# Optimization experiments

Hardware: AMD Instinct MI355X
Metric: run time of the kernel (lower is better)

The kernel has to match this reference:

```python
import jax, jax.numpy as jnp
import numpy as np

THRESHOLD = 0.5
VARIANCE = (0.1, 0.2)
ALPHA = 0.25
GAMMA = 2
NUM_CLASSES = 2
EPS = 1e-07


def _point_form(p):
    # center-form [cx,cy,w,h] -> corner-form [x0,y0,x1,y1]
    return jnp.concatenate([p[:, :2] - p[:, 2:] / 2, p[:, :2] + p[:, 2:] / 2], axis=1)


def _jaccard(a, b):
    # a: [O,4] corner-form truths, b: [P,4] corner-form priors -> IoU [O,P]
    lt = jnp.maximum(a[:, None, :2], b[None, :, :2])
    rb = jnp.minimum(a[:, None, 2:], b[None, :, 2:])
    wh = jnp.clip(rb - lt, 0.0)
    inter = wh[..., 0] * wh[..., 1]
    area_a = ((a[:, 2] - a[:, 0]) * (a[:, 3] - a[:, 1]))[:, None]
    area_b = ((b[:, 2] - b[:, 0]) * (b[:, 3] - b[:, 1]))[None, :]
    return inter / (area_a + area_b - inter)


def _encode(matched, priors):
    # matched: [P,4] corner-form GT, priors: [P,4] center-form
    g_cxcy = ((matched[:, :2] + matched[:, 2:]) / 2 - priors[:, :2]) / (VARIANCE[0] * priors[:, 2:])
    g_wh = jnp.log((matched[:, 2:] - matched[:, :2]) / priors[:, 2:]) / VARIANCE[1]
    return jnp.concatenate([g_cxcy, g_wh], axis=1)


def _match(truths, labels, priors):
    # truths: [O,4] corner-form, labels: [O], priors: [P,4] center-form
    overlaps = _jaccard(truths, _point_form(priors))            # [O,P]
    best_prior_idx = jnp.argmax(overlaps, axis=1)               # [O]
    best_truth_overlap = jnp.max(overlaps, axis=0)              # [P]
    best_truth_idx = jnp.argmax(overlaps, axis=0)               # [P]
    # guarantee each GT keeps its best prior
    best_truth_overlap = best_truth_overlap.at[best_prior_idx].set(2.0)
    best_truth_idx = best_truth_idx.at[best_prior_idx].set(jnp.arange(truths.shape[0]))
    matched = truths[best_truth_idx]                            # [P,4]
    conf = labels[best_truth_idx].astype(jnp.int32) + 1
    conf = jnp.where(best_truth_overlap < THRESHOLD, 0, conf)   # background -> 0
    loc = _encode(matched, priors)
    return loc, conf


def setup_inputs() -> dict:
    key = jax.random.key(0)
    k1, k2, k3, k4, k5, k6 = jax.random.split(key, 6)
    B, P, O = 128, 24564, 20
    loc_data = jax.random.normal(k1, (B, P, 4), dtype=jnp.float32)
    conf_data = jax.random.normal(k2, (B, P, NUM_CLASSES), dtype=jnp.float32)
    # priors in center-form with valid positive w,h
    cxcy = jax.random.uniform(k3, (P, 2), minval=0.05, maxval=0.95)
    wh = jax.random.uniform(k4, (P, 2), minval=0.05, maxval=0.3)
    priors = jnp.concatenate([cxcy, wh], axis=1).astype(jnp.float32)
    # GT boxes in corner-form + label column (single foreground class 0)
    gc = jax.random.uniform(k5, (B, O, 2), minval=0.15, maxval=0.85)
    gwh = jax.random.uniform(k6, (B, O, 2), minval=0.05, maxval=0.25)
    bbox_targets = jnp.concatenate(
        [gc - gwh / 2, gc + gwh / 2, jnp.zeros((B, O, 1))], axis=-1
    ).astype(jnp.float32)
    return {"loc_data": loc_data, "conf_data": conf_data, "priors": priors,
            "bbox_targets": bbox_targets}


def reference(loc_data, conf_data, priors, bbox_targets):
    # per-image matching, vectorized over the batch
    loc_t, conf_t = jax.vmap(lambda gt: _match(gt[:, :4], gt[:, 4], priors))(bbox_targets)
    loc_t = jax.lax.stop_gradient(loc_t)
    conf_t = jax.lax.stop_gradient(conf_t)

    pos = conf_t > 0                                             # [B,P]
    # smooth-L1 on positives (sum reduction); masking == dynamic gather + sum
    d = loc_data - loc_t
    ad = jnp.abs(d)
    sl1 = jnp.where(ad < 1.0, 0.5 * d * d, ad - 0.5)
    loss_l = jnp.sum(sl1 * pos[..., None].astype(sl1.dtype))

    # focal loss over pos+neg (conf_t > -1); torch one-hot via eye(2)
    pos_neg = conf_t > -1
    t = jax.nn.one_hot(conf_t, NUM_CLASSES, dtype=jnp.float32)   # [B,P,2]
    logit = jnp.clip(jax.nn.softmax(conf_data, axis=-1), EPS, 1.0 - EPS)
    fl = ALPHA * (-t * jnp.log(logit)) * (1.0 - logit) ** GAMMA
    loss_c = jnp.sum(fl * pos_neg[..., None].astype(fl.dtype))

    num_pos = jnp.maximum(1.0, jnp.sum(pos).astype(jnp.float32))
    return loss_l / num_pos, loss_c / num_pos
```

## Files before the change

kernel.cpp:

```cpp
#include <hip/hip_runtime.h>


#define NB 128
#define NP 24564
#define NO 20

#define IPT1 12
#define NCH1 8
#define NBLK1 (NB * NCH1)
#define NPART (NBLK1 + NB)

#define PK_OFF 0
#define PL_OFF ((size_t)NB * NO * 8)
#define PN_OFF (PL_OFF + (size_t)NPART * 8)
#define WS_NEEDED (PN_OFF + (size_t)NPART * 4)

__device__ __forceinline__ float fast_rcp(float x) {
    return __builtin_amdgcn_rcpf(x);
}

__device__ __forceinline__ float focal_term(float2 cd, int conf) {
    float mx = fmaxf(cd.x, cd.y);
    float e0 = __expf(cd.x - mx), e1 = __expf(cd.y - mx);
    if (conf > 1) return 0.0f;
    float pc = ((conf == 0) ? e0 : e1) * fast_rcp(e0 + e1);
    pc = fminf(fmaxf(pc, 1e-7f), 1.0f - 1e-7f);
    float om = 1.0f - pc;
    return 0.25f * (-__logf(pc)) * om * om;
}

__device__ __forceinline__ float sl1_term(float4 m, float4 pr, float4 ld) {
    float gx = ((m.x + m.z) * 0.5f - pr.x) / (0.1f * pr.z);
    float gy = ((m.y + m.w) * 0.5f - pr.y) / (0.1f * pr.w);
    float gw = logf((m.z - m.x) / pr.z) / 0.2f;
    float gh = logf((m.w - m.y) / pr.w) / 0.2f;
    float d0 = ld.x - gx, d1 = ld.y - gy, d2 = ld.z - gw, d3 = ld.w - gh;
    float a0 = fabsf(d0), a1 = fabsf(d1), a2 = fabsf(d2), a3 = fabsf(d3);
    float r = (a0 < 1.0f) ? 0.5f * d0 * d0 : a0 - 0.5f;
    r += (a1 < 1.0f) ? 0.5f * d1 * d1 : a1 - 0.5f;
    r += (a2 < 1.0f) ? 0.5f * d2 * d2 : a2 - 0.5f;
    r += (a3 < 1.0f) ? 0.5f * d3 * d3 : a3 - 0.5f;
    return r;
}

__global__ __launch_bounds__(256) void init_ws_kernel(unsigned long long* __restrict__ packed) {
    int i = blockIdx.x * 256 + threadIdx.x;
    if (i < NB * NO) packed[i] = 0ull;
}

__global__ __launch_bounds__(256) void match_loss_kernel(
    const float4* __restrict__ loc_data,
    const float2* __restrict__ conf_data,
    const float4* __restrict__ priors,
    const float* __restrict__ bbox,
    unsigned long long* __restrict__ packed,
    float2* __restrict__ part_loss,
    unsigned int* __restrict__ part_np)
{
    const int img  = blockIdx.x / NCH1;
    const int base = (blockIdx.x % NCH1) * (256 * IPT1);
    const int tid  = threadIdx.x;

    __shared__ float4 s_truth[NO];
    __shared__ float  s_area[NO];
    __shared__ int    s_label[NO];
    if (tid < NO) {
        const float* t = bbox + ((size_t)img * NO + tid) * 5;
        float4 tb = make_float4(t[0], t[1], t[2], t[3]);
        s_truth[tid] = tb;
        s_area[tid]  = (tb.z - tb.x) * (tb.w - tb.y);
        s_label[tid] = (int)t[4];
    }
    __syncthreads();

    float bf[NO];
    int   bk[NO];
#pragma unroll
    for (int o = 0; o < NO; ++o) { bf[o] = -1.0f; bk[o] = 0; }

    float lossl = 0.0f, lossc = 0.0f;
    int np = 0;

    for (int k = 0; k < IPT1; ++k) {
        const int p = base + k * 256 + tid;
        if (p >= NP) break;

        float4 pr = priors[p];
        float px0 = pr.x - pr.z * 0.5f, py0 = pr.y - pr.w * 0.5f;
        float px1 = pr.x + pr.z * 0.5f, py1 = pr.y + pr.w * 0.5f;
        float parea = (px1 - px0) * (py1 - py0);

        float bestv = -1.0f;
        int bi = 0;
#pragma unroll
        for (int o = 0; o < NO; ++o) {
            float4 tb = s_truth[o];
            float lx = fmaxf(tb.x, px0), ly = fmaxf(tb.y, py0);
            float rx = fminf(tb.z, px1), ry = fminf(tb.w, py1);
            float w = fmaxf(rx - lx, 0.0f);
            float h = fmaxf(ry - ly, 0.0f);
            float inter = w * h;
            float iou = inter * fast_rcp(s_area[o] + parea - inter);
            if (iou > bf[o]) { bf[o] = iou; bk[o] = k; }
            if (iou > bestv) { bestv = iou; bi = o; }
        }

        const int conf = (bestv >= 0.5f) ? (s_label[bi] + 1) : 0;
        if (conf > 0) {
            np++;
            lossl += sl1_term(s_truth[bi], pr, loc_data[(size_t)img * NP + p]);
        }
        lossc += focal_term(conf_data[(size_t)img * NP + p], conf);
    }

#pragma unroll
    for (int o = 0; o < NO; ++o) {
        const int p = base + bk[o] * 256 + tid;
        unsigned long long v = ((unsigned long long)__float_as_uint(bf[o]) << 32)
                             | (unsigned long long)(0xFFFFFFFFu - (unsigned)p);
#pragma unroll
        for (int s = 32; s > 0; s >>= 1) {
            unsigned long long u = __shfl_xor(v, s, 64);
            v = (v > u) ? v : u;
        }
        if ((tid & 63) == 0) atomicMax(&packed[img * NO + o], v);
    }

#pragma unroll
    for (int s = 32; s > 0; s >>= 1) {
        lossl += __shfl_xor(lossl, s, 64);
        lossc += __shfl_xor(lossc, s, 64);
        np    += __shfl_xor(np, s, 64);
    }
    __shared__ float s_ll[4], s_lc[4];
    __shared__ int s_np4[4];
    int wid = tid >> 6;
    if ((tid & 63) == 0) { s_ll[wid] = lossl; s_lc[wid] = lossc; s_np4[wid] = np; }
    __syncthreads();
    if (tid == 0) {
        float tl = 0.0f, tc = 0.0f;
        int tn = 0;
        for (int w = 0; w < 4; ++w) { tl += s_ll[w]; tc += s_lc[w]; tn += s_np4[w]; }
        part_loss[blockIdx.x] = make_float2(tl, tc);
        part_np[blockIdx.x]   = (unsigned int)tn;
    }
}

__global__ __launch_bounds__(64) void fixup_kernel(
    const float4* __restrict__ loc_data,
    const float2* __restrict__ conf_data,
    const float4* __restrict__ priors,
    const float* __restrict__ bbox,
    const unsigned long long* __restrict__ packed,
    float2* __restrict__ part_loss,
    unsigned int* __restrict__ part_np)
{
    const int img = blockIdx.x;
    const int o   = threadIdx.x;

    __shared__ float4 s_truth[NO];
    __shared__ float  s_area[NO];
    __shared__ int    s_label[NO];
    if (o < NO) {
        const float* t = bbox + ((size_t)img * NO + o) * 5;
        float4 tb = make_float4(t[0], t[1], t[2], t[3]);
        s_truth[o] = tb;
        s_area[o]  = (tb.z - tb.x) * (tb.w - tb.y);
        s_label[o] = (int)t[4];
    }
    __syncthreads();

    int bp = -1;
    if (o < NO) {
        unsigned long long v = packed[(size_t)img * NO + o];
        bp = (int)(0xFFFFFFFFu - (unsigned)(v & 0xFFFFFFFFull));
    }
    bool win = (o < NO);
#pragma unroll
    for (int o2 = 0; o2 < NO; ++o2) {
        int bp2 = __shfl(bp, o2, 64);
        if (o2 > o && bp2 == bp) win = false;
    }

    float dll = 0.0f, dlc = 0.0f;
    int dnp = 0;
    if (win) {
        float4 pr = priors[bp];
        float px0 = pr.x - pr.z * 0.5f, py0 = pr.y - pr.w * 0.5f;
        float px1 = pr.x + pr.z * 0.5f, py1 = pr.y + pr.w * 0.5f;
        float parea = (px1 - px0) * (py1 - py0);

        float bestv = -1.0f;
        int bi = 0;
#pragma unroll
        for (int o3 = 0; o3 < NO; ++o3) {
            float4 tb = s_truth[o3];
            float lx = fmaxf(tb.x, px0), ly = fmaxf(tb.y, py0);
            float rx = fminf(tb.z, px1), ry = fminf(tb.w, py1);
            float w = fmaxf(rx - lx, 0.0f);
            float h = fmaxf(ry - ly, 0.0f);
            float inter = w * h;
            float iou = inter * fast_rcp(s_area[o3] + parea - inter);
            if (iou > bestv) { bestv = iou; bi = o3; }
        }
        const int conf_old = (bestv >= 0.5f) ? (s_label[bi] + 1) : 0;
        const int conf_new = s_label[o] + 1;

        float2 cd = conf_data[(size_t)img * NP + bp];
        float4 ld = loc_data[(size_t)img * NP + bp];

        dlc = focal_term(cd, conf_new) - focal_term(cd, conf_old);
        float sl_new = sl1_term(s_truth[o], pr, ld);
        float sl_old = (conf_old > 0) ? sl1_term(s_truth[bi], pr, ld) : 0.0f;
        dll = sl_new - sl_old;
        dnp = (conf_old == 0) ? 1 : 0;
    }

#pragma unroll
    for (int s = 32; s > 0; s >>= 1) {
        dll += __shfl_xor(dll, s, 64);
        dlc += __shfl_xor(dlc, s, 64);
        dnp += __shfl_xor(dnp, s, 64);
    }
    if (o == 0) {
        part_loss[NBLK1 + img] = make_float2(dll, dlc);
        part_np[NBLK1 + img]   = (unsigned int)dnp;
    }
}

__global__ __launch_bounds__(256) void finalize_kernel(
    const float2* __restrict__ part_loss,
    const unsigned int* __restrict__ part_np,
    float* __restrict__ out)
{
    double ll = 0.0, lc = 0.0;
    unsigned int np = 0;
    for (int i = threadIdx.x; i < NPART; i += 256) {
        float2 v = part_loss[i];
        ll += (double)v.x;
        lc += (double)v.y;
        np += part_np[i];
    }
#pragma unroll
    for (int s = 32; s > 0; s >>= 1) {
        ll += __shfl_xor(ll, s, 64);
        lc += __shfl_xor(lc, s, 64);
        np += __shfl_xor(np, s, 64);
    }
    __shared__ double s_ll[4], s_lc[4];
    __shared__ unsigned int s_np4[4];
    int wid = threadIdx.x >> 6;
    if ((threadIdx.x & 63) == 0) { s_ll[wid] = ll; s_lc[wid] = lc; s_np4[wid] = np; }
    __syncthreads();
    if (threadIdx.x == 0) {
        double tl = 0.0, tc = 0.0;
        unsigned int tn = 0;
        for (int w = 0; w < 4; ++w) { tl += s_ll[w]; tc += s_lc[w]; tn += s_np4[w]; }
        double npd = (tn > 0u) ? (double)tn : 1.0;
        out[0] = (float)(tl / npd);
        out[1] = (float)(tc / npd);
    }
}

extern "C" void kernel_launch(void* const* d_in, const int* in_sizes, int n_in,
                              void* d_out, int out_size, void* d_ws, size_t ws_size,
                              hipStream_t stream) {
    const float4* loc_data  = (const float4*)d_in[0];
    const float2* conf_data = (const float2*)d_in[1];
    const float4* priors    = (const float4*)d_in[2];
    const float*  bbox      = (const float*)d_in[3];
    float* out = (float*)d_out;

    unsigned long long* packed = (unsigned long long*)((char*)d_ws + PK_OFF);
    float2* part_loss = (float2*)((char*)d_ws + PL_OFF);
    unsigned int* part_np = (unsigned int*)((char*)d_ws + PN_OFF);

    init_ws_kernel<<<(NB * NO + 255) / 256, 256, 0, stream>>>(packed);
    match_loss_kernel<<<NBLK1, 256, 0, stream>>>(loc_data, conf_data, priors, bbox,
                                                 packed, part_loss, part_np);
    fixup_kernel<<<NB, 64, 0, stream>>>(loc_data, conf_data, priors, bbox,
                                        packed, part_loss, part_np);
    finalize_kernel<<<1, 256, 0, stream>>>(part_loss, part_np, out);
}
```

Measured before the change: 181.7 us.

## Tile priors per thread, drop atomics, merge fixup and finalize into one kernel

The main matching loop now processes 4 priors per thread at once across each truth box, so every shared-memory truth load serves several IoU computations and more independent work is exposed. Per-truth best-prior keys are reduced within each block in shared memory and written per block, replacing the global atomicMax and removing the init kernel. The fixup and finalize kernels are fused into one single-block epilogue that reduces the per-block keys and applies all corrections, which cuts launches from four to two. The cost is a serial fixup loop over 20 truths in 128 threads of a single block, plus more register pressure from the tiling.

Result: slower. 279.9 us (+54.0%).

```diff
diff --git a/kernel.cpp b/kernel.cpp
--- a/kernel.cpp
+++ b/kernel.cpp
@@ -5,15 +5,16 @@
 #define NP 24564
 #define NO 20
 
-#define IPT1 12
+#define TILE 4
+#define NTILE 3
+#define IPT1 (TILE * NTILE)
 #define NCH1 8
+#define CHUNK (256 * IPT1)
 #define NBLK1 (NB * NCH1)
-#define NPART (NBLK1 + NB)
-
-#define PK_OFF 0
-#define PL_OFF ((size_t)NB * NO * 8)
-#define PN_OFF (PL_OFF + (size_t)NPART * 8)
-#define WS_NEEDED (PN_OFF + (size_t)NPART * 4)
+
+#define KEY_OFF 0
+#define PL_OFF  ((size_t)NBLK1 * NO * 8)
+#define PN_OFF  (PL_OFF + (size_t)NBLK1 * 8)
 
 __device__ __forceinline__ float fast_rcp(float x) {
     return __builtin_amdgcn_rcpf(x);
@@ -43,27 +44,24 @@
     return r;
 }
 
-__global__ __launch_bounds__(256) void init_ws_kernel(unsigned long long* __restrict__ packed) {
-    int i = blockIdx.x * 256 + threadIdx.x;
-    if (i < NB * NO) packed[i] = 0ull;
-}
-
 __global__ __launch_bounds__(256) void match_loss_kernel(
     const float4* __restrict__ loc_data,
     const float2* __restrict__ conf_data,
     const float4* __restrict__ priors,
     const float* __restrict__ bbox,
-    unsigned long long* __restrict__ packed,
+    unsigned long long* __restrict__ pb_keys,
     float2* __restrict__ part_loss,
     unsigned int* __restrict__ part_np)
 {
     const int img  = blockIdx.x / NCH1;
-    const int base = (blockIdx.x % NCH1) * (256 * IPT1);
+    const int base = (blockIdx.x % NCH1) * CHUNK;
     const int tid  = threadIdx.x;
 
     __shared__ float4 s_truth[NO];
     __shared__ float  s_area[NO];
     __shared__ int    s_label[NO];
+    __shared__ unsigned long long s_keys[4][NO];
+
     if (tid < NO) {
         const float* t = bbox + ((size_t)img * NO + tid) * 5;
         float4 tb = make_float4(t[0], t[1], t[2], t[3]);
@@ -81,36 +79,56 @@
     float lossl = 0.0f, lossc = 0.0f;
     int np = 0;
 
-    for (int k = 0; k < IPT1; ++k) {
-        const int p = base + k * 256 + tid;
-        if (p >= NP) break;
-
-        float4 pr = priors[p];
-        float px0 = pr.x - pr.z * 0.5f, py0 = pr.y - pr.w * 0.5f;
-        float px1 = pr.x + pr.z * 0.5f, py1 = pr.y + pr.w * 0.5f;
-        float parea = (px1 - px0) * (py1 - py0);
-
-        float bestv = -1.0f;
-        int bi = 0;
+    for (int t = 0; t < NTILE; ++t) {
+        float qx0[TILE], qy0[TILE], qx1[TILE], qy1[TILE], qa[TILE];
+        float bv[TILE];
+        int   bj[TILE];
+#pragma unroll
+        for (int j = 0; j < TILE; ++j) {
+            const int p = base + (t * TILE + j) * 256 + tid;
+            const bool valid = (p < NP);
+            float4 pr = priors[valid ? p : (NP - 1)];
+            float x0 = pr.x - pr.z * 0.5f, y0 = pr.y - pr.w * 0.5f;
+            float x1 = pr.x + pr.z * 0.5f, y1 = pr.y + pr.w * 0.5f;
+            qx0[j] = valid ? x0 : 3.0e18f;
+            qy0[j] = valid ? y0 : 3.0e18f;
+            qx1[j] = valid ? x1 : 3.0e18f;
+            qy1[j] = valid ? y1 : 3.0e18f;
+            qa[j]  = valid ? (x1 - x0) * (y1 - y0) : 0.0f;
+            bv[j] = -1.0f;
+            bj[j] = 0;
+        }
+
 #pragma unroll
         for (int o = 0; o < NO; ++o) {
-            float4 tb = s_truth[o];
-            float lx = fmaxf(tb.x, px0), ly = fmaxf(tb.y, py0);
-            float rx = fminf(tb.z, px1), ry = fminf(tb.w, py1);
-            float w = fmaxf(rx - lx, 0.0f);
-            float h = fmaxf(ry - ly, 0.0f);
-            float inter = w * h;
-            float iou = inter * fast_rcp(s_area[o] + parea - inter);
-            if (iou > bf[o]) { bf[o] = iou; bk[o] = k; }
-            if (iou > bestv) { bestv = iou; bi = o; }
-        }
-
-        const int conf = (bestv >= 0.5f) ? (s_label[bi] + 1) : 0;
-        if (conf > 0) {
-            np++;
-            lossl += sl1_term(s_truth[bi], pr, loc_data[(size_t)img * NP + p]);
-        }
-        lossc += focal_term(conf_data[(size_t)img * NP + p], conf);
+            const float4 tb = s_truth[o];
+            const float  ta = s_area[o];
+#pragma unroll
+            for (int j = 0; j < TILE; ++j) {
+                float lx = fmaxf(tb.x, qx0[j]), ly = fmaxf(tb.y, qy0[j]);
+                float rx = fminf(tb.z, qx1[j]), ry = fminf(tb.w, qy1[j]);
+                float w = fmaxf(rx - lx, 0.0f);
+                float h = fmaxf(ry - ly, 0.0f);
+                float inter = w * h;
+                float iou = inter * fast_rcp(ta + qa[j] - inter);
+                if (iou > bf[o]) { bf[o] = iou; bk[o] = t * TILE + j; }
+                if (iou > bv[j]) { bv[j] = iou; bj[j] = o; }
+            }
+        }
+
+#pragma unroll
+        for (int j = 0; j < TILE; ++j) {
+            const int p = base + (t * TILE + j) * 256 + tid;
+            if (p >= NP) continue;
+            const int conf = (bv[j] >= 0.5f) ? (s_label[bj[j]] + 1) : 0;
+            if (conf > 0) {
+                np++;
+                float4 pr = priors[p];
+                lossl += sl1_term(s_truth[bj[j]], pr,
+                                  loc_data[(size_t)img * NP + p]);
+            }
+            lossc += focal_term(conf_data[(size_t)img * NP + p], conf);
+        }
     }
 
 #pragma unroll
@@ -123,7 +141,7 @@
             unsigned long long u = __shfl_xor(v, s, 64);
             v = (v > u) ? v : u;
         }
-        if ((tid & 63) == 0) atomicMax(&packed[img * NO + o], v);
+        if ((tid & 63) == 0) s_keys[tid >> 6][o] = v;
     }
 
 #pragma unroll
@@ -134,9 +152,18 @@
     }
     __shared__ float s_ll[4], s_lc[4];
     __shared__ int s_np4[4];
-    int wid = tid >> 6;
+    const int wid = tid >> 6;
     if ((tid & 63) == 0) { s_ll[wid] = lossl; s_lc[wid] = lossc; s_np4[wid] = np; }
     __syncthreads();
+
+    if (tid < NO) {
+        unsigned long long m = s_keys[0][tid];
+        for (int w = 1; w < 4; ++w) {
+            unsigned long long u = s_keys[w][tid];
+            m = (m > u) ? m : u;
+        }
+        pb_keys[(size_t)blockIdx.x * NO + tid] = m;
+    }
     if (tid == 0) {
         float tl = 0.0f, tc = 0.0f;
         int tn = 0;
@@ -146,97 +173,90 @@
     }
 }
 
-__global__ __launch_bounds__(64) void fixup_kernel(
+#define TRS 101
+
+__global__ __launch_bounds__(256) void epilogue_kernel(
     const float4* __restrict__ loc_data,
     const float2* __restrict__ conf_data,
     const float4* __restrict__ priors,
     const float* __restrict__ bbox,
-    const unsigned long long* __restrict__ packed,
-    float2* __restrict__ part_loss,
-    unsigned int* __restrict__ part_np)
-{
-    const int img = blockIdx.x;
-    const int o   = threadIdx.x;
-
-    __shared__ float4 s_truth[NO];
-    __shared__ float  s_area[NO];
-    __shared__ int    s_label[NO];
-    if (o < NO) {
-        const float* t = bbox + ((size_t)img * NO + o) * 5;
-        float4 tb = make_float4(t[0], t[1], t[2], t[3]);
-        s_truth[o] = tb;
-        s_area[o]  = (tb.z - tb.x) * (tb.w - tb.y);
-        s_label[o] = (int)t[4];
-    }
-    __syncthreads();
-
-    int bp = -1;
-    if (o < NO) {
-        unsigned long long v = packed[(size_t)img * NO + o];
-        bp = (int)(0xFFFFFFFFu - (unsigned)(v & 0xFFFFFFFFull));
-    }
-    bool win = (o < NO);
-#pragma unroll
-    for (int o2 = 0; o2 < NO; ++o2) {
-        int bp2 = __shfl(bp, o2, 64);
-        if (o2 > o && bp2 == bp) win = false;
-    }
-
-    float dll = 0.0f, dlc = 0.0f;
-    int dnp = 0;
-    if (win) {
-        float4 pr = priors[bp];
-        float px0 = pr.x - pr.z * 0.5f, py0 = pr.y - pr.w * 0.5f;
-        float px1 = pr.x + pr.z * 0.5f, py1 = pr.y + pr.w * 0.5f;
-        float parea = (px1 - px0) * (py1 - py0);
-
-        float bestv = -1.0f;
-        int bi = 0;
-#pragma unroll
-        for (int o3 = 0; o3 < NO; ++o3) {
-            float4 tb = s_truth[o3];
-            float lx = fmaxf(tb.x, px0), ly = fmaxf(tb.y, py0);
-            float rx = fminf(tb.z, px1), ry = fminf(tb.w, py1);
-            float w = fmaxf(rx - lx, 0.0f);
-            float h = fmaxf(ry - ly, 0.0f);
-            float inter = w * h;
-            float iou = inter * fast_rcp(s_area[o3] + parea - inter);
-            if (iou > bestv) { bestv = iou; bi = o3; }
-        }
-        const int conf_old = (bestv >= 0.5f) ? (s_label[bi] + 1) : 0;
-        const int conf_new = s_label[o] + 1;
-
-        float2 cd = conf_data[(size_t)img * NP + bp];
-        float4 ld = loc_data[(size_t)img * NP + bp];
-
-        dlc = focal_term(cd, conf_new) - focal_term(cd, conf_old);
-        float sl_new = sl1_term(s_truth[o], pr, ld);
-        float sl_old = (conf_old > 0) ? sl1_term(s_truth[bi], pr, ld) : 0.0f;
-        dll = sl_new - sl_old;
-        dnp = (conf_old == 0) ? 1 : 0;
-    }
-
-#pragma unroll
-    for (int s = 32; s > 0; s >>= 1) {
-        dll += __shfl_xor(dll, s, 64);
-        dlc += __shfl_xor(dlc, s, 64);
-        dnp += __shfl_xor(dnp, s, 64);
-    }
-    if (o == 0) {
-        part_loss[NBLK1 + img] = make_float2(dll, dlc);
-        part_np[NBLK1 + img]   = (unsigned int)dnp;
-    }
-}
-
-__global__ __launch_bounds__(256) void finalize_kernel(
+    const unsigned long long* __restrict__ pb_keys,
     const float2* __restrict__ part_loss,
     const unsigned int* __restrict__ part_np,
     float* __restrict__ out)
 {
-    double ll = 0.0, lc = 0.0;
-    unsigned int np = 0;
-    for (int i = threadIdx.x; i < NPART; i += 256) {
-        float2 v = part_loss[i];
+    const int tid = threadIdx.x;
+    __shared__ float s_tr[NB * TRS];
+    __shared__ int   s_bp[NB][NO];
+
+    for (int i = tid; i < NB * NO * 5; i += 256) {
+        const int img = i / (NO * 5), f = i % (NO * 5);
+        s_tr[img * TRS + f] = bbox[i];
+    }
+    for (int u = tid; u < NB * NO; u += 256) {
+        const int img = u / NO, o = u - img * NO;
+        unsigned long long m = 0ull;
+        for (int c = 0; c < NCH1; ++c) {
+            unsigned long long v = pb_keys[((size_t)(img * NCH1 + c)) * NO + o];
+            m = (m > v) ? m : v;
+        }
+        s_bp[img][o] = (int)(0xFFFFFFFFu - (unsigned)(m & 0xFFFFFFFFull));
+    }
+    __syncthreads();
+
+    float dll = 0.0f, dlc = 0.0f;
+    int dnp = 0;
+    if (tid < NB) {
+        const int img = tid;
+        for (int o = 0; o < NO; ++o) {
+            const int bp = s_bp[img][o];
+            bool win = true;
+            for (int o2 = o + 1; o2 < NO; ++o2) win = win && (s_bp[img][o2] != bp);
+            if (!win) continue;
+
+            float4 pr = priors[bp];
+            const float px0 = pr.x - pr.z * 0.5f, py0 = pr.y - pr.w * 0.5f;
+            const float px1 = pr.x + pr.z * 0.5f, py1 = pr.y + pr.w * 0.5f;
+            const float parea = (px1 - px0) * (py1 - py0);
+
+            float bestv = -1.0f;
+            int bi = 0;
+            for (int o3 = 0; o3 < NO; ++o3) {
+                const float* tp = &s_tr[img * TRS + o3 * 5];
+                const float tx0 = tp[0], ty0 = tp[1], tx1 = tp[2], ty1 = tp[3];
+                const float ta = (tx1 - tx0) * (ty1 - ty0);
+                float lx = fmaxf(tx0, px0), ly = fmaxf(ty0, py0);
+                float rx = fminf(tx1, px1), ry = fminf(ty1, py1);
+                float w = fmaxf(rx - lx, 0.0f);
+                float h = fmaxf(ry - ly, 0.0f);
+                float inter = w * h;
+                float iou = inter * fast_rcp(ta + parea - inter);
+                if (iou > bestv) { bestv = iou; bi = o3; }
+            }
+            const int conf_old = (bestv >= 0.5f)
+                               ? ((int)s_tr[img * TRS + bi * 5 + 4] + 1) : 0;
+            const int conf_new = (int)s_tr[img * TRS + o * 5 + 4] + 1;
+
+            const float2 cd = conf_data[(size_t)img * NP + bp];
+            const float4 ld = loc_data[(size_t)img * NP + bp];
+
+            dlc += focal_term(cd, conf_new) - focal_term(cd, conf_old);
+            const float* tn_ = &s_tr[img * TRS + o * 5];
+            float sl_new = sl1_term(make_float4(tn_[0], tn_[1], tn_[2], tn_[3]), pr, ld);
+            float sl_old = 0.0f;
+            if (conf_old > 0) {
+                const float* to_ = &s_tr[img * TRS + bi * 5];
+                sl_old = sl1_term(make_float4(to_[0], to_[1], to_[2], to_[3]), pr, ld);
+            }
+            dll += sl_new - sl_old;
+            dnp += (conf_old == 0) ? 1 : 0;
+        }
+    }
+
+    double ll = (double)dll, lc = (double)dlc;
+    unsigned int np = (unsigned int)dnp;
+    for (int i = tid; i < NBLK1; i += 256) {
+        const float2 v = part_loss[i];
         ll += (double)v.x;
         lc += (double)v.y;
         np += part_np[i];
@@ -247,16 +267,16 @@
         lc += __shfl_xor(lc, s, 64);
         np += __shfl_xor(np, s, 64);
     }
-    __shared__ double s_ll[4], s_lc[4];
-    __shared__ unsigned int s_np4[4];
-    int wid = threadIdx.x >> 6;
-    if ((threadIdx.x & 63) == 0) { s_ll[wid] = ll; s_lc[wid] = lc; s_np4[wid] = np; }
+    __shared__ double r_ll[4], r_lc[4];
+    __shared__ unsigned int r_np[4];
+    const int wid = tid >> 6;
+    if ((tid & 63) == 0) { r_ll[wid] = ll; r_lc[wid] = lc; r_np[wid] = np; }
     __syncthreads();
-    if (threadIdx.x == 0) {
+    if (tid == 0) {
         double tl = 0.0, tc = 0.0;
         unsigned int tn = 0;
-        for (int w = 0; w < 4; ++w) { tl += s_ll[w]; tc += s_lc[w]; tn += s_np4[w]; }
-        double npd = (tn > 0u) ? (double)tn : 1.0;
+        for (int w = 0; w < 4; ++w) { tl += r_ll[w]; tc += r_lc[w]; tn += r_np[w]; }
+        const double npd = (tn > 0u) ? (double)tn : 1.0;
         out[0] = (float)(tl / npd);
         out[1] = (float)(tc / npd);
     }
@@ -271,14 +291,12 @@
     const float*  bbox      = (const float*)d_in[3];
     float* out = (float*)d_out;
 
-    unsigned long long* packed = (unsigned long long*)((char*)d_ws + PK_OFF);
+    unsigned long long* pb_keys = (unsigned long long*)((char*)d_ws + KEY_OFF);
     float2* part_loss = (float2*)((char*)d_ws + PL_OFF);
     unsigned int* part_np = (unsigned int*)((char*)d_ws + PN_OFF);
 
-    init_ws_kernel<<<(NB * NO + 255) / 256, 256, 0, stream>>>(packed);
     match_loss_kernel<<<NBLK1, 256, 0, stream>>>(loc_data, conf_data, priors, bbox,
-                                                 packed, part_loss, part_np);
-    fixup_kernel<<<NB, 64, 0, stream>>>(loc_data, conf_data, priors, bbox,
-                                        packed, part_loss, part_np);
-    finalize_kernel<<<1, 256, 0, stream>>>(part_loss, part_np, out);
-}
+                                                 pb_keys, part_loss, part_np);
+    epilogue_kernel<<<1, 256, 0, stream>>>(loc_data, conf_data, priors, bbox,
+                                           pb_keys, part_loss, part_np, out);
+}
```
